# Optimization experiments

Hardware: AMD Instinct MI355X
Metric: run time of the kernel (lower is better)

Reference implementation:

```python
import jax, jax.numpy as jnp
import numpy as np


def setup_inputs() -> dict:
    key = jax.random.key(0)
    ks = jax.random.split(key, 6)
    B, H, W, C = 8, 128, 128, 256
    x = jax.random.normal(ks[0], (B, H, W), dtype=jnp.float32)
    atten_x_full = jax.random.normal(ks[1], (B, H, W, W), dtype=jnp.float32)
    atten_y_full = jax.random.normal(ks[2], (B, W, H, H), dtype=jnp.float32)
    value_full = jax.random.normal(ks[3], (B, H, W, C), dtype=jnp.float32)
    # nn.Parameter init: shift = |randn|, bias = -|randn|
    shift = jnp.abs(jax.random.normal(ks[4], (1,), dtype=jnp.float32))
    bias = -jnp.abs(jax.random.normal(ks[5], (1,), dtype=jnp.float32))
    return {"x": x, "atten_x_full": atten_x_full, "atten_y_full": atten_y_full,
            "value_full": value_full, "shift": shift, "bias": bias}


def reference(x, atten_x_full, atten_y_full, value_full, shift, bias):
    H, W = x.shape[1], x.shape[2]
    # Gaussian distance biases: gx[c, h] = -(shift*(h-c)^2 + bias), gy[r, w] likewise
    hw = jnp.arange(W, dtype=jnp.float32)
    hh = jnp.arange(H, dtype=jnp.float32)
    gx = -(shift[0] * (hw[None, :] - hw[:, None]) ** 2 + bias[0])  # [W, W]
    gy = -(shift[0] * (hh[None, :] - hh[:, None]) ** 2 + bias[0])  # [H, H]
    # atten_x_full indexed [b, r, c, k] -> add gx[c, k]; softmax over k (row direction)
    Ax = jax.nn.softmax(atten_x_full + gx[None, None, :, :], axis=-1)  # [B,H,W,W]
    # atten_y_full indexed [b, c, r, k] -> add gy[r, k]; softmax over k (col direction)
    Ay = jax.nn.softmax(atten_y_full + gy[None, None, :, :], axis=-1)  # [B,W,H,H]
    out = (jnp.einsum('brck,brkd->brcd', Ax, value_full)
           + jnp.einsum('bcrk,bkcd->brcd', Ay, value_full))  # [B,H,W,C]
    return out
```

## Files before the change

### kernel.cpp

```cpp
#include <hip/hip_runtime.h>
#include <hip/hip_bf16.h>

typedef __attribute__((ext_vector_type(8))) short short8;
typedef __attribute__((ext_vector_type(4))) float floatx4;
typedef __attribute__((ext_vector_type(2))) float floatx2;

#define LDK 136

__device__ __forceinline__ unsigned short f2bf(float x) {
    unsigned u = __builtin_bit_cast(unsigned, x);
    return (unsigned short)((u + 0x7fffu + ((u >> 16) & 1u)) >> 16);
}

template <bool ACCUM>
__global__ __launch_bounds__(512) void gtrans(
    const float* __restrict__ atten, const float* __restrict__ value,
    float* __restrict__ out, const float* __restrict__ shiftp,
    const float* __restrict__ biasp, int s0, int s1)
{
    __shared__ short Buf[128 * LDK];

    const int bi   = blockIdx.x;
    const int b    = bi >> 7;
    const int i    = bi & 127;
    const int tid  = threadIdx.x;
    const int lane = tid & 63;
    const int w    = tid >> 6;

    const float shift = shiftp[0];
    const float bias  = biasp[0];

    const float* abase = atten + (size_t)bi * (128 * 128);
    const float* vbase = value + (size_t)b * (128 * 128 * 256) + (size_t)i * s0;
    float*       obase = out   + (size_t)b * (128 * 128 * 256) + (size_t)i * s0;

    {
        floatx2 v[16];
#pragma unroll
        for (int j = 0; j < 16; ++j) {
            int c = w * 16 + j;
            v[j] = *(const floatx2*)(abase + c * 128 + 2 * lane);
        }
#pragma unroll
        for (int j = 0; j < 16; ++j) {
            int c = w * 16 + j;
            float d0 = (float)(2 * lane)     - (float)c;
            float d1 = (float)(2 * lane + 1) - (float)c;
            float a0 = v[j].x - (shift * d0 * d0 + bias);
            float a1 = v[j].y - (shift * d1 * d1 + bias);
            float m = fmaxf(a0, a1);
#pragma unroll
            for (int s = 1; s < 64; s <<= 1) m = fmaxf(m, __shfl_xor(m, s, 64));
            float e0 = __expf(a0 - m);
            float e1 = __expf(a1 - m);
            float ssum = e0 + e1;
#pragma unroll
            for (int s = 1; s < 64; s <<= 1) ssum += __shfl_xor(ssum, s, 64);
            float r = 1.0f / ssum;
            unsigned p = (unsigned)f2bf(e0 * r) | ((unsigned)f2bf(e1 * r) << 16);
            *(unsigned*)(&Buf[c * LDK + 2 * lane]) = p;
        }
    }
    __syncthreads();

    short8 bfrag[4];
    {
        int n  = w * 16 + (lane & 15);
        int kq = (lane >> 4) * 8;
#pragma unroll
        for (int ks = 0; ks < 4; ++ks)
            bfrag[ks] = *(const short8*)(&Buf[n * LDK + ks * 32 + kq]);
    }
    __syncthreads();

    floatx4 acc[8];
    const int am = lane & 15;
    const int kq = (lane >> 4) * 8;
#pragma unroll
    for (int half = 0; half < 2; ++half) {
        {
            floatx2 vv[16];
#pragma unroll
            for (int j = 0; j < 16; ++j) {
                int k = w * 16 + j;
                vv[j] = *(const floatx2*)(vbase + (size_t)k * s1 + half * 128 + 2 * lane);
            }
#pragma unroll
            for (int j = 0; j < 16; ++j) {
                int k  = w * 16 + j;
                int dl = 2 * lane;
                Buf[dl * LDK + k]       = (short)f2bf(vv[j].x);
                Buf[(dl + 1) * LDK + k] = (short)f2bf(vv[j].y);
            }
        }
        __syncthreads();

#pragma unroll
        for (int t = 0; t < 8; ++t) acc[t] = (floatx4)0.0f;

#pragma unroll
        for (int ks = 0; ks < 4; ++ks) {
#pragma unroll
            for (int t = 0; t < 8; ++t) {
                short8 af = *(const short8*)(&Buf[(t * 16 + am) * LDK + ks * 32 + kq]);
                acc[t] = __builtin_amdgcn_mfma_f32_16x16x32_bf16(af, bfrag[ks], acc[t], 0, 0, 0);
            }
        }

        {
            int n = w * 16 + (lane & 15);
            float* orow = obase + (size_t)n * s1 + half * 128 + (lane >> 4) * 4;
#pragma unroll
            for (int t = 0; t < 8; ++t) {
                float* p = orow + t * 16;
                floatx4 res = acc[t];
                if (ACCUM) {
                    floatx4 old = *(const floatx4*)p;
                    res = res + old;
                }
                *(floatx4*)p = res;
            }
        }
        __syncthreads();
    }
}

extern "C" void kernel_launch(void* const* d_in, const int* in_sizes, int n_in,
                              void* d_out, int out_size, void* d_ws, size_t ws_size,
                              hipStream_t stream) {
    const float* atten_x = (const float*)d_in[1];
    const float* atten_y = (const float*)d_in[2];
    const float* value   = (const float*)d_in[3];
    const float* shiftp  = (const float*)d_in[4];
    const float* biasp   = (const float*)d_in[5];
    float* out = (float*)d_out;

    dim3 grid(1024), block(512);
    gtrans<false><<<grid, block, 0, stream>>>(atten_x, value, out, shiftp, biasp,
                                              128 * 256, 256);
    gtrans<true><<<grid, block, 0, stream>>>(atten_y, value, out, shiftp, biasp,
                                             256, 128 * 256);
}
```

Baseline: 410.1 us.

## Prefetch value halves into registers, widen loads, drop redundant barriers

Attention rows are now loaded as float4 and each softmax row is reduced across 32 lanes instead of 64. The value tile is loaded with float4 reads and written to shared memory as packed 32-bit transposed pairs instead of scattered 16-bit stores. The second half of the value tile is prefetched into registers while the first half's MFMAs run. Two barriers are removed because each wavefront only touches its own softmax rows. Launch bounds now request 4 blocks per CU, which caps register use and may cause spills in exchange for higher occupancy on a mostly bandwidth-bound kernel.

```diff
diff --git a/kernel.cpp b/kernel.cpp
--- a/kernel.cpp
+++ b/kernel.cpp
@@ -3,7 +3,6 @@
 
 typedef __attribute__((ext_vector_type(8))) short short8;
 typedef __attribute__((ext_vector_type(4))) float floatx4;
-typedef __attribute__((ext_vector_type(2))) float floatx2;
 
 #define LDK 136
 
@@ -13,7 +12,7 @@
 }
 
 template <bool ACCUM>
-__global__ __launch_bounds__(512) void gtrans(
+__global__ __launch_bounds__(512, 4) void gtrans(
     const float* __restrict__ atten, const float* __restrict__ value,
     float* __restrict__ out, const float* __restrict__ shiftp,
     const float* __restrict__ biasp, int s0, int s1)
@@ -34,94 +33,129 @@
     const float* vbase = value + (size_t)b * (128 * 128 * 256) + (size_t)i * s0;
     float*       obase = out   + (size_t)b * (128 * 128 * 256) + (size_t)i * s0;
 
+    const int k0   = 2 * lane;
+    const int dw   = 16 * w;
+    const int rofs = lane >> 5;
+    const int acol = 4 * (lane & 31);
+
+    floatx4 aA[8];
+#pragma unroll
+    for (int j = 0; j < 8; ++j)
+        aA[j] = *(const floatx4*)(abase + (dw + 2 * j + rofs) * 128 + acol);
+
+    floatx4 aV[8];
     {
-        floatx2 v[16];
+        const float* vp = vbase + (size_t)k0 * s1 + dw;
 #pragma unroll
-        for (int j = 0; j < 16; ++j) {
-            int c = w * 16 + j;
-            v[j] = *(const floatx2*)(abase + c * 128 + 2 * lane);
+        for (int q = 0; q < 4; ++q) aV[q]     = *(const floatx4*)(vp + 4 * q);
+#pragma unroll
+        for (int q = 0; q < 4; ++q) aV[4 + q] = *(const floatx4*)(vp + s1 + 4 * q);
+    }
+
+#pragma unroll
+    for (int j = 0; j < 8; ++j) {
+        const int c = dw + 2 * j + rofs;
+        const float cf = (float)c;
+        float a[4];
+#pragma unroll
+        for (int e = 0; e < 4; ++e) {
+            float d = (float)(acol + e) - cf;
+            a[e] = aA[j][e] - (shift * d * d + bias);
         }
+        float mx = fmaxf(fmaxf(a[0], a[1]), fmaxf(a[2], a[3]));
 #pragma unroll
-        for (int j = 0; j < 16; ++j) {
-            int c = w * 16 + j;
-            float d0 = (float)(2 * lane)     - (float)c;
-            float d1 = (float)(2 * lane + 1) - (float)c;
-            float a0 = v[j].x - (shift * d0 * d0 + bias);
-            float a1 = v[j].y - (shift * d1 * d1 + bias);
-            float m = fmaxf(a0, a1);
+        for (int s = 1; s < 32; s <<= 1) mx = fmaxf(mx, __shfl_xor(mx, s, 32));
+        float e0 = __expf(a[0] - mx), e1 = __expf(a[1] - mx);
+        float e2 = __expf(a[2] - mx), e3 = __expf(a[3] - mx);
+        float ssum = (e0 + e1) + (e2 + e3);
 #pragma unroll
-            for (int s = 1; s < 64; s <<= 1) m = fmaxf(m, __shfl_xor(m, s, 64));
-            float e0 = __expf(a0 - m);
-            float e1 = __expf(a1 - m);
-            float ssum = e0 + e1;
-#pragma unroll
-            for (int s = 1; s < 64; s <<= 1) ssum += __shfl_xor(ssum, s, 64);
-            float r = 1.0f / ssum;
-            unsigned p = (unsigned)f2bf(e0 * r) | ((unsigned)f2bf(e1 * r) << 16);
-            *(unsigned*)(&Buf[c * LDK + 2 * lane]) = p;
-        }
+        for (int s = 1; s < 32; s <<= 1) ssum += __shfl_xor(ssum, s, 32);
+        float r = 1.0f / ssum;
+        unsigned long long p =
+              (unsigned long long)f2bf(e0 * r)
+            | ((unsigned long long)f2bf(e1 * r) << 16)
+            | ((unsigned long long)f2bf(e2 * r) << 32)
+            | ((unsigned long long)f2bf(e3 * r) << 48);
+        *(unsigned long long*)(&Buf[c * LDK + acol]) = p;
     }
-    __syncthreads();
 
     short8 bfrag[4];
+    const int am = lane & 15;
+    const int kq = (lane >> 4) * 8;
     {
-        int n  = w * 16 + (lane & 15);
-        int kq = (lane >> 4) * 8;
+        const int n = dw + am;
 #pragma unroll
         for (int ks = 0; ks < 4; ++ks)
             bfrag[ks] = *(const short8*)(&Buf[n * LDK + ks * 32 + kq]);
     }
+
+#pragma unroll
+    for (int j = 0; j < 16; ++j) {
+        unsigned lo = f2bf(aV[j >> 2][j & 3]);
+        unsigned hi = f2bf(aV[4 + (j >> 2)][j & 3]);
+        *(unsigned*)(&Buf[(dw + j) * LDK + k0]) = lo | (hi << 16);
+    }
+
+    {
+        const float* vp = vbase + (size_t)k0 * s1 + 128 + dw;
+#pragma unroll
+        for (int q = 0; q < 4; ++q) aV[q]     = *(const floatx4*)(vp + 4 * q);
+#pragma unroll
+        for (int q = 0; q < 4; ++q) aV[4 + q] = *(const floatx4*)(vp + s1 + 4 * q);
+    }
+
     __syncthreads();
 
     floatx4 acc[8];
-    const int am = lane & 15;
-    const int kq = (lane >> 4) * 8;
 #pragma unroll
-    for (int half = 0; half < 2; ++half) {
-        {
-            floatx2 vv[16];
+    for (int t = 0; t < 8; ++t) acc[t] = (floatx4)0.0f;
 #pragma unroll
-            for (int j = 0; j < 16; ++j) {
-                int k = w * 16 + j;
-                vv[j] = *(const floatx2*)(vbase + (size_t)k * s1 + half * 128 + 2 * lane);
-            }
+    for (int ks = 0; ks < 4; ++ks)
 #pragma unroll
-            for (int j = 0; j < 16; ++j) {
-                int k  = w * 16 + j;
-                int dl = 2 * lane;
-                Buf[dl * LDK + k]       = (short)f2bf(vv[j].x);
-                Buf[(dl + 1) * LDK + k] = (short)f2bf(vv[j].y);
-            }
+        for (int t = 0; t < 8; ++t) {
+            short8 af = *(const short8*)(&Buf[(t * 16 + am) * LDK + ks * 32 + kq]);
+            acc[t] = __builtin_amdgcn_mfma_f32_16x16x32_bf16(af, bfrag[ks], acc[t], 0, 0, 0);
         }
-        __syncthreads();
+
+    __syncthreads();
 
 #pragma unroll
-        for (int t = 0; t < 8; ++t) acc[t] = (floatx4)0.0f;
+    for (int j = 0; j < 16; ++j) {
+        unsigned lo = f2bf(aV[j >> 2][j & 3]);
+        unsigned hi = f2bf(aV[4 + (j >> 2)][j & 3]);
+        *(unsigned*)(&Buf[(dw + j) * LDK + k0]) = lo | (hi << 16);
+    }
+    {
+        float* orow = obase + (size_t)(dw + am) * s1 + (lane >> 4) * 4;
+#pragma unroll
+        for (int t = 0; t < 8; ++t) {
+            float* p = orow + t * 16;
+            floatx4 res = acc[t];
+            if (ACCUM) res = res + *(const floatx4*)p;
+            *(floatx4*)p = res;
+        }
+    }
+
+    __syncthreads();
 
 #pragma unroll
-        for (int ks = 0; ks < 4; ++ks) {
+    for (int t = 0; t < 8; ++t) acc[t] = (floatx4)0.0f;
 #pragma unroll
-            for (int t = 0; t < 8; ++t) {
-                short8 af = *(const short8*)(&Buf[(t * 16 + am) * LDK + ks * 32 + kq]);
-                acc[t] = __builtin_amdgcn_mfma_f32_16x16x32_bf16(af, bfrag[ks], acc[t], 0, 0, 0);
-            }
+    for (int ks = 0; ks < 4; ++ks)
+#pragma unroll
+        for (int t = 0; t < 8; ++t) {
+            short8 af = *(const short8*)(&Buf[(t * 16 + am) * LDK + ks * 32 + kq]);
+            acc[t] = __builtin_amdgcn_mfma_f32_16x16x32_bf16(af, bfrag[ks], acc[t], 0, 0, 0);
         }
-
-        {
-            int n = w * 16 + (lane & 15);
-            float* orow = obase + (size_t)n * s1 + half * 128 + (lane >> 4) * 4;
+    {
+        float* orow = obase + (size_t)(dw + am) * s1 + 128 + (lane >> 4) * 4;
 #pragma unroll
-            for (int t = 0; t < 8; ++t) {
-                float* p = orow + t * 16;
-                floatx4 res = acc[t];
-                if (ACCUM) {
-                    floatx4 old = *(const floatx4*)p;
-                    res = res + old;
-                }
-                *(floatx4*)p = res;
-            }
+        for (int t = 0; t < 8; ++t) {
+            float* p = orow + t * 16;
+            floatx4 res = acc[t];
+            if (ACCUM) res = res + *(const floatx4*)p;
+            *(floatx4*)p = res;
         }
-        __syncthreads();
     }
 }
 
```

Result: no change. 417.0 us (+1.7%).

## Load attention fragments directly to registers and stage full value tile once

Applied to the files above, without the earlier changes.

Each wave now loads its attention rows straight into the MFMA B-fragment layout and computes the softmax in registers with 2-step shuffles, so the LDS round trip for probabilities is gone. The full 256-column value tile is loaded up front and transposed into dynamic LDS in one pass, which removes the two-half loop and most of the barriers. Accumulate-mode output reads are prefetched one group ahead, and launch bounds request 4 waves per SIMD. The cost is a doubled LDS footprint (about 69 KB per block) and higher register pressure, which may limit occupancy.

```diff
diff --git a/kernel.cpp b/kernel.cpp
--- a/kernel.cpp
+++ b/kernel.cpp
@@ -1,24 +1,27 @@
 #include <hip/hip_runtime.h>
-#include <hip/hip_bf16.h>
 
 typedef __attribute__((ext_vector_type(8))) short short8;
 typedef __attribute__((ext_vector_type(4))) float floatx4;
-typedef __attribute__((ext_vector_type(2))) float floatx2;
 
 #define LDK 136
+#define LDS_BYTES (256 * LDK * 2)
 
-__device__ __forceinline__ unsigned short f2bf(float x) {
+__device__ __forceinline__ unsigned f2bf1(float x) {
     unsigned u = __builtin_bit_cast(unsigned, x);
-    return (unsigned short)((u + 0x7fffu + ((u >> 16) & 1u)) >> 16);
+    return (u + 0x7fffu + ((u >> 16) & 1u)) >> 16;
+}
+__device__ __forceinline__ unsigned packbf(float lo, float hi) {
+    return f2bf1(lo) | (f2bf1(hi) << 16);
 }
 
 template <bool ACCUM>
-__global__ __launch_bounds__(512) void gtrans(
+__global__ __launch_bounds__(512, 4) void gtrans(
     const float* __restrict__ atten, const float* __restrict__ value,
     float* __restrict__ out, const float* __restrict__ shiftp,
     const float* __restrict__ biasp, int s0, int s1)
 {
-    __shared__ short Buf[128 * LDK];
+    extern __shared__ short Buf[];
+    unsigned* Buf32 = (unsigned*)Buf;
 
     const int bi   = blockIdx.x;
     const int b    = bi >> 7;
@@ -34,94 +37,126 @@
     const float* vbase = value + (size_t)b * (128 * 128 * 256) + (size_t)i * s0;
     float*       obase = out   + (size_t)b * (128 * 128 * 256) + (size_t)i * s0;
 
+    const int rrow = 16 * w + (lane & 15);
+    const int kq8  = (lane >> 4) * 8;
+    const int k0   = 16 * w + 2 * (lane >> 3);
+    const int d0   = 4 * (lane & 7);
+
+    floatx4 aA[8];
+#pragma unroll
+    for (int ks = 0; ks < 4; ++ks) {
+        const float* ap = abase + rrow * 128 + ks * 32 + kq8;
+        aA[2 * ks]     = *(const floatx4*)(ap);
+        aA[2 * ks + 1] = *(const floatx4*)(ap + 4);
+    }
+    floatx4 va[8], vb[8];
     {
-        floatx2 v[16];
+        const float* vp0 = vbase + (size_t)k0 * s1 + d0;
+        const float* vp1 = vp0 + s1;
 #pragma unroll
-        for (int j = 0; j < 16; ++j) {
-            int c = w * 16 + j;
-            v[j] = *(const floatx2*)(abase + c * 128 + 2 * lane);
+        for (int q = 0; q < 8; ++q) va[q] = *(const floatx4*)(vp0 + 32 * q);
+#pragma unroll
+        for (int q = 0; q < 8; ++q) vb[q] = *(const floatx4*)(vp1 + 32 * q);
+    }
+    __builtin_amdgcn_sched_barrier(0);
+
+    floatx4 e8[8];
+    {
+        float mx = -1e30f;
+#pragma unroll
+        for (int j = 0; j < 8; ++j) {
+            const int kb = (j >> 1) * 32 + kq8 + (j & 1) * 4;
+            floatx4 v = aA[j];
+            floatx4 t;
+#pragma unroll
+            for (int e = 0; e < 4; ++e) {
+                float d = (float)(kb + e - rrow);
+                t[e] = v[e] - (shift * d * d + bias);
+            }
+            e8[j] = t;
+            mx = fmaxf(mx, fmaxf(fmaxf(t[0], t[1]), fmaxf(t[2], t[3])));
+        }
+        mx = fmaxf(mx, __shfl_xor(mx, 16, 64));
+        mx = fmaxf(mx, __shfl_xor(mx, 32, 64));
+        float ssum = 0.0f;
+#pragma unroll
+        for (int j = 0; j < 8; ++j) {
+            floatx4 t = e8[j];
+#pragma unroll
+            for (int e = 0; e < 4; ++e) t[e] = __expf(t[e] - mx);
+            e8[j] = t;
+            ssum += (t[0] + t[1]) + (t[2] + t[3]);
+        }
+        ssum += __shfl_xor(ssum, 16, 64);
+        ssum += __shfl_xor(ssum, 32, 64);
+        float r = 1.0f / ssum;
+#pragma unroll
+        for (int j = 0; j < 8; ++j) {
+#pragma unroll
+            for (int e = 0; e < 4; ++e) e8[j][e] *= r;
+        }
+    }
+
+    short8 bfrag[4];
+#pragma unroll
+    for (int ks = 0; ks < 4; ++ks) {
+        union { short8 s; unsigned u[4]; } uu;
+        floatx4 lo = e8[2 * ks], hi = e8[2 * ks + 1];
+        uu.u[0] = packbf(lo[0], lo[1]);
+        uu.u[1] = packbf(lo[2], lo[3]);
+        uu.u[2] = packbf(hi[0], hi[1]);
+        uu.u[3] = packbf(hi[2], hi[3]);
+        bfrag[ks] = uu.s;
+    }
+
+#pragma unroll
+    for (int q = 0; q < 8; ++q)
+#pragma unroll
+        for (int e = 0; e < 4; ++e)
+            Buf32[(d0 + 32 * q + e) * (LDK / 2) + (k0 >> 1)] = packbf(va[q][e], vb[q][e]);
+
+    const int dq = 4 * (lane >> 4);
+    float* orow = obase + (size_t)rrow * s1 + dq;
+    floatx4 aO[4];
+    if (ACCUM) {
+#pragma unroll
+        for (int t = 0; t < 4; ++t) aO[t] = *(const floatx4*)(orow + t * 16);
+    }
+
+    __builtin_amdgcn_sched_barrier(0);
+    asm volatile("s_waitcnt lgkmcnt(0)" ::: "memory");
+    __builtin_amdgcn_s_barrier();
+
+#pragma unroll
+    for (int g = 0; g < 4; ++g) {
+        floatx4 aN[4];
+        if (ACCUM && g < 3) {
+#pragma unroll
+            for (int t = 0; t < 4; ++t)
+                aN[t] = *(const floatx4*)(orow + (g + 1) * 64 + t * 16);
+        }
+        floatx4 acc[4];
+#pragma unroll
+        for (int t = 0; t < 4; ++t) acc[t] = (floatx4)0.0f;
+#pragma unroll
+        for (int tt = 0; tt < 4; ++tt) {
+            const short* base = &Buf[((g * 4 + tt) * 16 + (lane & 15)) * LDK + kq8];
+#pragma unroll
+            for (int ks = 0; ks < 4; ++ks) {
+                short8 af = *(const short8*)(base + ks * 32);
+                acc[tt] = __builtin_amdgcn_mfma_f32_16x16x32_bf16(af, bfrag[ks], acc[tt], 0, 0, 0);
+            }
         }
 #pragma unroll
-        for (int j = 0; j < 16; ++j) {
-            int c = w * 16 + j;
-            float d0 = (float)(2 * lane)     - (float)c;
-            float d1 = (float)(2 * lane + 1) - (float)c;
-            float a0 = v[j].x - (shift * d0 * d0 + bias);
-            float a1 = v[j].y - (shift * d1 * d1 + bias);
-            float m = fmaxf(a0, a1);
+        for (int t = 0; t < 4; ++t) {
+            floatx4 res = acc[t];
+            if (ACCUM) res = res + aO[t];
+            *(floatx4*)(orow + g * 64 + t * 16) = res;
+        }
+        if (ACCUM && g < 3) {
 #pragma unroll
-            for (int s = 1; s < 64; s <<= 1) m = fmaxf(m, __shfl_xor(m, s, 64));
-            float e0 = __expf(a0 - m);
-            float e1 = __expf(a1 - m);
-            float ssum = e0 + e1;
-#pragma unroll
-            for (int s = 1; s < 64; s <<= 1) ssum += __shfl_xor(ssum, s, 64);
-            float r = 1.0f / ssum;
-            unsigned p = (unsigned)f2bf(e0 * r) | ((unsigned)f2bf(e1 * r) << 16);
-            *(unsigned*)(&Buf[c * LDK + 2 * lane]) = p;
+            for (int t = 0; t < 4; ++t) aO[t] = aN[t];
         }
-    }
-    __syncthreads();
-
-    short8 bfrag[4];
-    {
-        int n  = w * 16 + (lane & 15);
-        int kq = (lane >> 4) * 8;
-#pragma unroll
-        for (int ks = 0; ks < 4; ++ks)
-            bfrag[ks] = *(const short8*)(&Buf[n * LDK + ks * 32 + kq]);
-    }
-    __syncthreads();
-
-    floatx4 acc[8];
-    const int am = lane & 15;
-    const int kq = (lane >> 4) * 8;
-#pragma unroll
-    for (int half = 0; half < 2; ++half) {
-        {
-            floatx2 vv[16];
-#pragma unroll
-            for (int j = 0; j < 16; ++j) {
-                int k = w * 16 + j;
-                vv[j] = *(const floatx2*)(vbase + (size_t)k * s1 + half * 128 + 2 * lane);
-            }
-#pragma unroll
-            for (int j = 0; j < 16; ++j) {
-                int k  = w * 16 + j;
-                int dl = 2 * lane;
-                Buf[dl * LDK + k]       = (short)f2bf(vv[j].x);
-                Buf[(dl + 1) * LDK + k] = (short)f2bf(vv[j].y);
-            }
-        }
-        __syncthreads();
-
-#pragma unroll
-        for (int t = 0; t < 8; ++t) acc[t] = (floatx4)0.0f;
-
-#pragma unroll
-        for (int ks = 0; ks < 4; ++ks) {
-#pragma unroll
-            for (int t = 0; t < 8; ++t) {
-                short8 af = *(const short8*)(&Buf[(t * 16 + am) * LDK + ks * 32 + kq]);
-                acc[t] = __builtin_amdgcn_mfma_f32_16x16x32_bf16(af, bfrag[ks], acc[t], 0, 0, 0);
-            }
-        }
-
-        {
-            int n = w * 16 + (lane & 15);
-            float* orow = obase + (size_t)n * s1 + half * 128 + (lane >> 4) * 4;
-#pragma unroll
-            for (int t = 0; t < 8; ++t) {
-                float* p = orow + t * 16;
-                floatx4 res = acc[t];
-                if (ACCUM) {
-                    floatx4 old = *(const floatx4*)p;
-                    res = res + old;
-                }
-                *(floatx4*)p = res;
-            }
-        }
-        __syncthreads();
     }
 }
 
@@ -135,9 +170,18 @@
     const float* biasp   = (const float*)d_in[5];
     float* out = (float*)d_out;
 
+    static bool inited = false;
+    if (!inited) {
+        hipFuncSetAttribute((const void*)&gtrans<false>,
+                            hipFuncAttributeMaxDynamicSharedMemorySize, LDS_BYTES);
+        hipFuncSetAttribute((const void*)&gtrans<true>,
+                            hipFuncAttributeMaxDynamicSharedMemorySize, LDS_BYTES);
+        inited = true;
+    }
+
     dim3 grid(1024), block(512);
-    gtrans<false><<<grid, block, 0, stream>>>(atten_x, value, out, shiftp, biasp,
-                                              128 * 256, 256);
-    gtrans<true><<<grid, block, 0, stream>>>(atten_y, value, out, shiftp, biasp,
-                                             256, 128 * 256);
+    gtrans<false><<<grid, block, LDS_BYTES, stream>>>(atten_x, value, out, shiftp, biasp,
+                                                      128 * 256, 256);
+    gtrans<true><<<grid, block, LDS_BYTES, stream>>>(atten_y, value, out, shiftp, biasp,
+                                                     256, 128 * 256);
 }
```

Measured after the change: 409.4 us. About the same (-0.2%).
